# Optimization experiments

Hardware: AMD Instinct MI355X
Metric: run time of the kernel (lower is better)

The kernel has to match this reference:

```python
import jax, jax.numpy as jnp
import numpy as np

N_NODES = 100000


def _gcn_layer(h_in, W, b, src, dst, n_nodes):
    """PyG GCNConv: out = D^{-1/2} (A + I) D^{-1/2} (h_in @ W) + b.
    src/dst already include self-loops. Messages flow src -> dst."""
    h = h_in @ W  # [N, C_out]
    ones = jnp.ones(dst.shape[0], dtype=h.dtype)
    deg = jax.ops.segment_sum(ones, dst, num_segments=n_nodes)  # in-degree incl. self-loops
    dinv = jnp.where(deg > 0, jax.lax.rsqrt(deg), 0.0)
    norm = dinv[src] * dinv[dst]  # [E]
    msg = norm[:, None] * h[src]  # gather + scale, [E, C_out]
    out = jax.ops.segment_sum(msg, dst, num_segments=n_nodes)
    return out + b


def setup_inputs() -> dict:
    key = jax.random.key(0)
    ks = jax.random.split(key, 4)
    d_in, d_hid = 64, 64
    n_edges = 1600000
    x = jax.random.normal(ks[0], (N_NODES, d_in), dtype=jnp.float32)
    edge_index = jax.random.randint(ks[1], (2, n_edges), 0, N_NODES, dtype=jnp.int64)
    W1 = jax.random.normal(ks[2], (d_in, d_hid), dtype=jnp.float32) * (1.0 / np.sqrt(d_in))
    b1 = jnp.zeros((d_hid,), dtype=jnp.float32)
    W2 = jax.random.normal(ks[3], (d_hid, d_hid), dtype=jnp.float32) * (1.0 / np.sqrt(d_hid))
    b2 = jnp.zeros((d_hid,), dtype=jnp.float32)
    return {"x": x, "edge_index": edge_index, "W1": W1, "b1": b1, "W2": W2, "b2": b2}


def reference(x, edge_index, W1, b1, W2, b2):
    n = x.shape[0]
    loop = jnp.arange(n, dtype=edge_index.dtype)
    src = jnp.concatenate([edge_index[0], loop])  # add self-loops once, reused by both layers
    dst = jnp.concatenate([edge_index[1], loop])
    h = jax.nn.relu(_gcn_layer(x, W1, b1, src, dst, n))
    h = jax.nn.relu(_gcn_layer(h, W2, b2, src, dst, n))
    return h
```

## Files before the change

### kernel.cpp

```cpp
#include <hip/hip_runtime.h>
#include <hip/hip_bf16.h>


#define NDIM 64
#define BSHIFT 9
#define BNODES (1 << BSHIFT)
#define BCAP 10240
#define CHUNK 4096
#define CAPC 64
#define CSHIFT 6
#define MAXCHUNK 512
#define PHASES 13
#define PSHIFT 13

typedef float v2f __attribute__((ext_vector_type(2)));
typedef __attribute__((ext_vector_type(8))) short short8b;
typedef __attribute__((ext_vector_type(4))) float f32x4;

__device__ __forceinline__ unsigned f2bf_rne(float f) {
  unsigned u = __float_as_uint(f);
  return (u + 0x7fffu + ((u >> 16) & 1u)) >> 16;
}

__global__ __launch_bounds__(256) void bin_scatter_kernel(
    const int* __restrict__ src, const int* __restrict__ dst,
    unsigned* __restrict__ binned, int* __restrict__ cnt,
    int nedges, int nchunk, int nbuck) {
  __shared__ int lcnt[256], lbase[256], lcur[256], tscan[256];
  __shared__ int2 stage[CHUNK];
  const int t = threadIdx.x;
  const int c = blockIdx.x;
  const int i0 = c * CHUNK;
  int iend = i0 + CHUNK; if (iend > nedges) iend = nedges;
  lcnt[t] = 0;
  __syncthreads();
  for (int i = i0 + t; i < iend; i += 256)
    atomicAdd(&lcnt[dst[i] >> BSHIFT], 1);
  __syncthreads();
  tscan[t] = lcnt[t];
  __syncthreads();
  for (int off = 1; off < 256; off <<= 1) {
    int tv = (t >= off) ? tscan[t - off] : 0;
    __syncthreads();
    tscan[t] += tv;
    __syncthreads();
  }
  lbase[t] = tscan[t] - lcnt[t];
  lcur[t] = lbase[t];
  __syncthreads();
  for (int i = i0 + t; i < iend; i += 256) {
    int s = src[i], d = dst[i];
    int p = atomicAdd(&lcur[d >> BSHIFT], 1);
    stage[p] = make_int2(s, d);
  }
  __syncthreads();
  const int m = iend - i0;
  for (int i = t; i < m; i += 256) {
    int2 pr = stage[i];
    int b = pr.y >> BSHIFT;
    int off = i - lbase[b];
    if (off < CAPC)
      binned[(((size_t)b * nchunk + c) << CSHIFT) + off] =
          (((unsigned)(pr.y & (BNODES - 1))) << 17) | (unsigned)pr.x;
  }
  if (t < nbuck) cnt[t * nchunk + c] = (lcnt[t] < CAPC) ? lcnt[t] : CAPC;
}

struct CsrSh {
  int deg[BNODES], rpl[BNODES], tscan[256], ccnt[MAXCHUNK];
  int pcnt[BNODES * PHASES];
};
union CsrGemmSh {
  CsrSh c;
  ushort g[4][16 * NDIM];
};

__global__ __launch_bounds__(256) void csr_gemm1_kernel(
    const unsigned* __restrict__ binned, const int* __restrict__ cnt,
    int* __restrict__ rowbeg, int* __restrict__ rowend,
    int* __restrict__ csr_src, float* __restrict__ dinv,
    const float* __restrict__ X, const float* __restrict__ W,
    ushort* __restrict__ hsb, int n, int nchunk) {
  __shared__ __align__(16) CsrGemmSh sh;
  const int b = blockIdx.x, t = threadIdx.x;
  const int node0 = b << BSHIFT;
  int ncnt = n - node0; if (ncnt > BNODES) ncnt = BNODES;
  const int e0 = b * BCAP;
  const size_t bbase = ((size_t)b * nchunk) << CSHIFT;
  const int nslot = nchunk << CSHIFT;

  for (int i = t; i < BNODES * PHASES; i += 256) sh.c.pcnt[i] = 0;
  for (int i = t; i < nchunk; i += 256) sh.c.ccnt[i] = cnt[b * nchunk + i];
  __syncthreads();
  for (int idx = t; idx < nslot; idx += 256) {
    if ((idx & (CAPC - 1)) < sh.c.ccnt[idx >> CSHIFT]) {
      unsigned u = binned[bbase + idx];
      atomicAdd(&sh.c.pcnt[(u >> 17) * PHASES + ((u & 0x1FFFFu) >> PSHIFT)], 1);
    }
  }
  __syncthreads();
  for (int i = t; i < BNODES; i += 256) {
    int s = 0;
#pragma unroll
    for (int p = 0; p < PHASES; ++p) {
      int c = sh.c.pcnt[i * PHASES + p];
      sh.c.pcnt[i * PHASES + p] = s;
      s += c;
    }
    sh.c.deg[i] = s;
  }
  __syncthreads();
  int d0 = sh.c.deg[2 * t], d1 = sh.c.deg[2 * t + 1];
  int ps = d0 + d1;
  sh.c.tscan[t] = ps;
  __syncthreads();
  for (int off = 1; off < 256; off <<= 1) {
    int tv = (t >= off) ? sh.c.tscan[t - off] : 0;
    __syncthreads();
    sh.c.tscan[t] += tv;
    __syncthreads();
  }
  int eb = sh.c.tscan[t] - ps;
  sh.c.rpl[2 * t] = eb;
  sh.c.rpl[2 * t + 1] = eb + d0;
  __syncthreads();
  for (int i = t; i < ncnt; i += 256) {
    rowbeg[node0 + i] = e0 + sh.c.rpl[i];
    rowend[node0 + i] = e0 + sh.c.rpl[i] + sh.c.deg[i];
    dinv[node0 + i] = rsqrtf((float)sh.c.deg[i] + 1.0f);
  }
  __syncthreads();
  for (int idx = t; idx < nslot; idx += 256) {
    if ((idx & (CAPC - 1)) < sh.c.ccnt[idx >> CSHIFT]) {
      unsigned u = binned[bbase + idx];
      int nd = u >> 17;
      int s = (int)(u & 0x1FFFFu);
      int pos = sh.c.rpl[nd] + atomicAdd(&sh.c.pcnt[nd * PHASES + (s >> PSHIFT)], 1);
      csr_src[e0 + pos] = s;
    }
  }
  __syncthreads();

  const int l = t & 63;
  const int wv = t >> 6;
  const int lrow = l & 15;
  const int kg = l >> 4;
  short8b Whi[4][2], Wlo[4][2];
#pragma unroll
  for (int ct = 0; ct < 4; ++ct) {
#pragma unroll
    for (int ks = 0; ks < 2; ++ks) {
      const int c = ct * 16 + lrow;
      const int k0 = ks * 32 + kg * 8;
#pragma unroll
      for (int i = 0; i < 8; ++i) {
        float w = W[(k0 + i) * NDIM + c];
        unsigned hb = f2bf_rne(w);
        float hf = __uint_as_float(hb << 16);
        Whi[ct][ks][i] = (short)hb;
        Wlo[ct][ks][i] = (short)f2bf_rne(w - hf);
      }
    }
  }
  const int ntile = (ncnt + 15) >> 4;
  for (int ti = wv; ti < ntile; ti += 4) {
    const int row0 = node0 + (ti << 4);
    const int r = row0 + lrow;
    short8b Ahi[2], Alo[2];
    const float4* Xf = (const float4*)X;
#pragma unroll
    for (int ks = 0; ks < 2; ++ks) {
      float4 xa = make_float4(0.f, 0.f, 0.f, 0.f);
      float4 xb = make_float4(0.f, 0.f, 0.f, 0.f);
      if (r < n) {
        xa = Xf[(size_t)r * 16 + ks * 8 + kg * 2];
        xb = Xf[(size_t)r * 16 + ks * 8 + kg * 2 + 1];
      }
      float xs[8] = {xa.x, xa.y, xa.z, xa.w, xb.x, xb.y, xb.z, xb.w};
#pragma unroll
      for (int i = 0; i < 8; ++i) {
        unsigned hb = f2bf_rne(xs[i]);
        float hf = __uint_as_float(hb << 16);
        Ahi[ks][i] = (short)hb;
        Alo[ks][i] = (short)f2bf_rne(xs[i] - hf);
      }
    }
    f32x4 acc[4];
#pragma unroll
    for (int ct = 0; ct < 4; ++ct) {
      f32x4 a = {0.f, 0.f, 0.f, 0.f};
#pragma unroll
      for (int ks = 0; ks < 2; ++ks) {
        a = __builtin_amdgcn_mfma_f32_16x16x32_bf16(Ahi[ks], Whi[ct][ks], a, 0, 0, 0);
        a = __builtin_amdgcn_mfma_f32_16x16x32_bf16(Ahi[ks], Wlo[ct][ks], a, 0, 0, 0);
        a = __builtin_amdgcn_mfma_f32_16x16x32_bf16(Alo[ks], Whi[ct][ks], a, 0, 0, 0);
      }
      acc[ct] = a;
    }
#pragma unroll
    for (int q = 0; q < 4; ++q) {
      const int rr = row0 + kg * 4 + q;
      const float di = (rr < n) ? dinv[rr] : 0.f;
#pragma unroll
      for (int ct = 0; ct < 4; ++ct)
        sh.g[wv][(kg * 4 + q) * NDIM + ct * 16 + lrow] =
            (ushort)f2bf_rne(acc[ct][q] * di);
    }
#pragma unroll
    for (int e = 0; e < 2; ++e) {
      const int idx = e * 64 + l;
      const int rw = idx >> 3;
      if (row0 + rw < n)
        ((uint4*)hsb)[(size_t)(row0 + rw) * 8 + (idx & 7)] =
            ((const uint4*)sh.g[wv])[idx];
    }
  }
}

__global__ __launch_bounds__(256) void gemm_mfma_bf16_kernel(
    const ushort* __restrict__ Xin, const float* __restrict__ W,
    const float* __restrict__ dinv, ushort* __restrict__ hsb, int nrows) {
  __shared__ __attribute__((aligned(16))) ushort stage[4][16 * NDIM];
  const int tid = threadIdx.x;
  const int l = tid & 63;
  const int wv = tid >> 6;
  const int lrow = l & 15;
  const int kg = l >> 4;

  short8b Whi[4][2], Wlo[4][2];
#pragma unroll
  for (int ct = 0; ct < 4; ++ct) {
#pragma unroll
    for (int ks = 0; ks < 2; ++ks) {
      const int c = ct * 16 + lrow;
      const int k0 = ks * 32 + kg * 8;
#pragma unroll
      for (int i = 0; i < 8; ++i) {
        float w = W[(k0 + i) * NDIM + c];
        unsigned hb = f2bf_rne(w);
        float hf = __uint_as_float(hb << 16);
        Whi[ct][ks][i] = (short)hb;
        Wlo[ct][ks][i] = (short)f2bf_rne(w - hf);
      }
    }
  }

  const int tiles = (nrows + 15) >> 4;
  for (int tb = blockIdx.x * 4; tb < tiles; tb += gridDim.x * 4) {
    const int t = tb + wv;
    const int row0 = t << 4;
    const int r = row0 + lrow;
    short8b Ahi[2];
    const uint4* Xb = (const uint4*)Xin;
#pragma unroll
    for (int ks = 0; ks < 2; ++ks) {
      uint4 q = make_uint4(0u, 0u, 0u, 0u);
      if (r < nrows) q = Xb[(size_t)r * 8 + ks * 4 + kg];
      union { uint4 u; short8b s; } cv; cv.u = q;
      Ahi[ks] = cv.s;
    }
    f32x4 acc[4];
#pragma unroll
    for (int ct = 0; ct < 4; ++ct) {
      f32x4 a = {0.f, 0.f, 0.f, 0.f};
#pragma unroll
      for (int ks = 0; ks < 2; ++ks) {
        a = __builtin_amdgcn_mfma_f32_16x16x32_bf16(Ahi[ks], Whi[ct][ks], a, 0, 0, 0);
        a = __builtin_amdgcn_mfma_f32_16x16x32_bf16(Ahi[ks], Wlo[ct][ks], a, 0, 0, 0);
      }
      acc[ct] = a;
    }
#pragma unroll
    for (int q = 0; q < 4; ++q) {
      const int rr = row0 + kg * 4 + q;
      const float di = (rr < nrows) ? dinv[rr] : 0.f;
#pragma unroll
      for (int ct = 0; ct < 4; ++ct)
        stage[wv][(kg * 4 + q) * NDIM + ct * 16 + lrow] =
            (ushort)f2bf_rne(acc[ct][q] * di);
    }
    __syncthreads();
#pragma unroll
    for (int e = 0; e < 2; ++e) {
      const int idx = e * 64 + l;
      const int rw = idx >> 3;
      if (row0 + rw < nrows)
        ((uint4*)hsb)[(size_t)(row0 + rw) * 8 + (idx & 7)] =
            ((const uint4*)stage[wv])[idx];
    }
    __syncthreads();
  }
}

__device__ __forceinline__ void add8(v2f* acc, uint4 q) {
  v2f a0, a1, a2, a3;
  a0.x = __uint_as_float(q.x << 16); a0.y = __uint_as_float(q.x & 0xffff0000u);
  a1.x = __uint_as_float(q.y << 16); a1.y = __uint_as_float(q.y & 0xffff0000u);
  a2.x = __uint_as_float(q.z << 16); a2.y = __uint_as_float(q.z & 0xffff0000u);
  a3.x = __uint_as_float(q.w << 16); a3.y = __uint_as_float(q.w & 0xffff0000u);
  acc[0] += a0; acc[1] += a1; acc[2] += a2; acc[3] += a3;
}

template <bool BF16OUT>
__global__ __launch_bounds__(256) void agg_epi_kernel(
    const int* __restrict__ rowbeg, const int* __restrict__ rowend,
    const int* __restrict__ csr_src, const uint4* __restrict__ hsb4,
    const float* __restrict__ dinv, const float4* __restrict__ b4,
    void* __restrict__ outp, int n) {
  const int l = threadIdx.x & 63;
  const int wv = threadIdx.x >> 6;
  const int ql = l & 15;
  const int sg = ql >> 3;
  const int g = ql & 7;
  const int node = blockIdx.x * 16 + wv * 4 + (l >> 4);
  const bool alive = node < n;
  const int nodec = alive ? node : 0;
  int beg = rowbeg[nodec], end = rowend[nodec];
  if (!alive) { beg = 0; end = 0; }
  const int deg = end - beg;
  int dmax = deg;
  dmax = max(dmax, __shfl_xor(dmax, 16));
  dmax = max(dmax, __shfl_xor(dmax, 32));

  v2f acc[4];
#pragma unroll
  for (int i = 0; i < 4; ++i) acc[i] = (v2f)(0.f);

  for (int base = 0; base < dmax; base += 16) {
    const int rem = deg - base;
    int eidx = (ql < rem) ? csr_src[beg + base + ql] : 0;
#pragma unroll
    for (int j = 0; j < 16; j += 2) {
      const int e = j + sg;
      int s = __shfl(eidx, (l & 48) + e);
      uint4 q = hsb4[(size_t)s * 8 + g];
      if (e < rem) add8(acc, q);
    }
  }
  if (sg == 0) add8(acc, hsb4[(size_t)nodec * 8 + g]);

  float a[8];
#pragma unroll
  for (int i = 0; i < 4; ++i) { a[2 * i] = acc[i].x; a[2 * i + 1] = acc[i].y; }
#pragma unroll
  for (int i = 0; i < 8; ++i) a[i] += __shfl_xor(a[i], 8);

  if (sg == 0 && alive) {
    float di = dinv[node];
    float4 bb0 = b4[2 * g], bb1 = b4[2 * g + 1];
    float o[8];
    o[0] = fmaxf(di * a[0] + bb0.x, 0.f);
    o[1] = fmaxf(di * a[1] + bb0.y, 0.f);
    o[2] = fmaxf(di * a[2] + bb0.z, 0.f);
    o[3] = fmaxf(di * a[3] + bb0.w, 0.f);
    o[4] = fmaxf(di * a[4] + bb1.x, 0.f);
    o[5] = fmaxf(di * a[5] + bb1.y, 0.f);
    o[6] = fmaxf(di * a[6] + bb1.z, 0.f);
    o[7] = fmaxf(di * a[7] + bb1.w, 0.f);
    if (BF16OUT) {
      uint4 wvv;
      wvv.x = f2bf_rne(o[0]) | (f2bf_rne(o[1]) << 16);
      wvv.y = f2bf_rne(o[2]) | (f2bf_rne(o[3]) << 16);
      wvv.z = f2bf_rne(o[4]) | (f2bf_rne(o[5]) << 16);
      wvv.w = f2bf_rne(o[6]) | (f2bf_rne(o[7]) << 16);
      ((uint4*)outp)[(size_t)node * 8 + g] = wvv;
    } else {
      float4 o0 = make_float4(o[0], o[1], o[2], o[3]);
      float4 o1 = make_float4(o[4], o[5], o[6], o[7]);
      ((float4*)outp)[(size_t)node * 16 + 2 * g] = o0;
      ((float4*)outp)[(size_t)node * 16 + 2 * g + 1] = o1;
    }
  }
}

extern "C" void kernel_launch(void* const* d_in, const int* in_sizes, int n_in,
                              void* d_out, int out_size, void* d_ws, size_t ws_size,
                              hipStream_t stream) {
  const float* x  = (const float*)d_in[0];
  const int* eidx = (const int*)d_in[1];
  const float* W1 = (const float*)d_in[2];
  const float* b1 = (const float*)d_in[3];
  const float* W2 = (const float*)d_in[4];
  const float* b2 = (const float*)d_in[5];
  float* out = (float*)d_out;

  const int N = in_sizes[0] / NDIM;
  const int E = in_sizes[1] / 2;
  const int* src = eidx;
  const int* dst = eidx + E;
  const int NV = N * NDIM;
  const int nbuck = (N + BNODES - 1) >> BSHIFT;
  const int nchunk = (E + CHUNK - 1) / CHUNK;

  auto al128 = [](size_t v) { return (v + 127) & ~(size_t)127; };
  char* w = (char*)d_ws;
  unsigned* binned = (unsigned*)w;  w += al128(((size_t)nbuck * nchunk) << (CSHIFT + 2));
  int*   cnt     = (int*)w;    w += al128((size_t)nbuck * nchunk * 4);
  int*   csr_src = (int*)w;    w += al128((size_t)nbuck * BCAP * 4);
  int*   rowbeg  = (int*)w;    w += al128((size_t)N * 4);
  int*   rowend  = (int*)w;    w += al128((size_t)N * 4);
  float* dinv    = (float*)w;  w += al128((size_t)N * 4);
  ushort* hsb = (ushort*)w;  w += al128((size_t)NV * 2);
  ushort* h2b = (ushort*)w;

  bin_scatter_kernel<<<nchunk, 256, 0, stream>>>(src, dst, binned, cnt,
                                                 E, nchunk, nbuck);
  csr_gemm1_kernel<<<nbuck, 256, 0, stream>>>(binned, cnt, rowbeg, rowend,
                                              csr_src, dinv, x, W1, hsb,
                                              N, nchunk);
  agg_epi_kernel<true><<<(N + 15) / 16, 256, 0, stream>>>(
      rowbeg, rowend, csr_src, (const uint4*)hsb, dinv, (const float4*)b1, h2b, N);
  gemm_mfma_bf16_kernel<<<512, 256, 0, stream>>>(h2b, W2, dinv, hsb, N);
  agg_epi_kernel<false><<<(N + 15) / 16, 256, 0, stream>>>(
      rowbeg, rowend, csr_src, (const uint4*)hsb, dinv, (const float4*)b2, out, N);
}
```

Before: 260.0 us.

## Fuse binning, CSR build and first GEMM into one cooperative kernel

Merges the bin-scatter kernel and the CSR+GEMM1 kernel into a single persistent cooperative kernel that uses grid-wide syncs between phases, which removes a kernel launch boundary. The CSR phase now walks each chunk's valid entries serially per thread rather than striding over every slot, and GEMM1 tiles are spread across the whole grid instead of one bucket per block. In exchange it adds two grid syncs and a grid sized to occupancy (at most 512 blocks), so the binning and CSR phases loop over chunks and buckets. The per-thread serial chunk loops may also load-balance worse than before.

```diff
diff --git a/kernel.cpp b/kernel.cpp
--- a/kernel.cpp
+++ b/kernel.cpp
@@ -1,5 +1,8 @@
 #include <hip/hip_runtime.h>
+#include <hip/hip_cooperative_groups.h>
 #include <hip/hip_bf16.h>
+
+namespace cg = cooperative_groups;
 
 
 #define NDIM 64
@@ -22,127 +25,135 @@
   return (u + 0x7fffu + ((u >> 16) & 1u)) >> 16;
 }
 
-__global__ __launch_bounds__(256) void bin_scatter_kernel(
-    const int* __restrict__ src, const int* __restrict__ dst,
-    unsigned* __restrict__ binned, int* __restrict__ cnt,
-    int nedges, int nchunk, int nbuck) {
-  __shared__ int lcnt[256], lbase[256], lcur[256], tscan[256];
-  __shared__ int2 stage[CHUNK];
-  const int t = threadIdx.x;
-  const int c = blockIdx.x;
-  const int i0 = c * CHUNK;
-  int iend = i0 + CHUNK; if (iend > nedges) iend = nedges;
-  lcnt[t] = 0;
-  __syncthreads();
-  for (int i = i0 + t; i < iend; i += 256)
-    atomicAdd(&lcnt[dst[i] >> BSHIFT], 1);
-  __syncthreads();
-  tscan[t] = lcnt[t];
-  __syncthreads();
-  for (int off = 1; off < 256; off <<= 1) {
-    int tv = (t >= off) ? tscan[t - off] : 0;
-    __syncthreads();
-    tscan[t] += tv;
-    __syncthreads();
-  }
-  lbase[t] = tscan[t] - lcnt[t];
-  lcur[t] = lbase[t];
-  __syncthreads();
-  for (int i = i0 + t; i < iend; i += 256) {
-    int s = src[i], d = dst[i];
-    int p = atomicAdd(&lcur[d >> BSHIFT], 1);
-    stage[p] = make_int2(s, d);
-  }
-  __syncthreads();
-  const int m = iend - i0;
-  for (int i = t; i < m; i += 256) {
-    int2 pr = stage[i];
-    int b = pr.y >> BSHIFT;
-    int off = i - lbase[b];
-    if (off < CAPC)
-      binned[(((size_t)b * nchunk + c) << CSHIFT) + off] =
-          (((unsigned)(pr.y & (BNODES - 1))) << 17) | (unsigned)pr.x;
-  }
-  if (t < nbuck) cnt[t * nchunk + c] = (lcnt[t] < CAPC) ? lcnt[t] : CAPC;
-}
-
+struct BinSh {
+  int lcnt[256], lbase[256], lcur[256], tscan[256];
+  int2 stage[CHUNK];
+};
 struct CsrSh {
   int deg[BNODES], rpl[BNODES], tscan[256], ccnt[MAXCHUNK];
   int pcnt[BNODES * PHASES];
 };
-union CsrGemmSh {
+union FrontSh {
+  BinSh b;
   CsrSh c;
   ushort g[4][16 * NDIM];
 };
 
-__global__ __launch_bounds__(256) void csr_gemm1_kernel(
-    const unsigned* __restrict__ binned, const int* __restrict__ cnt,
+__global__ __launch_bounds__(256) void front_kernel(
+    const int* __restrict__ src, const int* __restrict__ dst,
+    unsigned* __restrict__ binned, int* __restrict__ cnt,
     int* __restrict__ rowbeg, int* __restrict__ rowend,
     int* __restrict__ csr_src, float* __restrict__ dinv,
     const float* __restrict__ X, const float* __restrict__ W,
-    ushort* __restrict__ hsb, int n, int nchunk) {
-  __shared__ __align__(16) CsrGemmSh sh;
-  const int b = blockIdx.x, t = threadIdx.x;
-  const int node0 = b << BSHIFT;
-  int ncnt = n - node0; if (ncnt > BNODES) ncnt = BNODES;
-  const int e0 = b * BCAP;
-  const size_t bbase = ((size_t)b * nchunk) << CSHIFT;
-  const int nslot = nchunk << CSHIFT;
-
-  for (int i = t; i < BNODES * PHASES; i += 256) sh.c.pcnt[i] = 0;
-  for (int i = t; i < nchunk; i += 256) sh.c.ccnt[i] = cnt[b * nchunk + i];
-  __syncthreads();
-  for (int idx = t; idx < nslot; idx += 256) {
-    if ((idx & (CAPC - 1)) < sh.c.ccnt[idx >> CSHIFT]) {
-      unsigned u = binned[bbase + idx];
-      atomicAdd(&sh.c.pcnt[(u >> 17) * PHASES + ((u & 0x1FFFFu) >> PSHIFT)], 1);
-    }
-  }
-  __syncthreads();
-  for (int i = t; i < BNODES; i += 256) {
-    int s = 0;
-#pragma unroll
-    for (int p = 0; p < PHASES; ++p) {
-      int c = sh.c.pcnt[i * PHASES + p];
-      sh.c.pcnt[i * PHASES + p] = s;
-      s += c;
-    }
-    sh.c.deg[i] = s;
-  }
-  __syncthreads();
-  int d0 = sh.c.deg[2 * t], d1 = sh.c.deg[2 * t + 1];
-  int ps = d0 + d1;
-  sh.c.tscan[t] = ps;
-  __syncthreads();
-  for (int off = 1; off < 256; off <<= 1) {
-    int tv = (t >= off) ? sh.c.tscan[t - off] : 0;
-    __syncthreads();
-    sh.c.tscan[t] += tv;
-    __syncthreads();
-  }
-  int eb = sh.c.tscan[t] - ps;
-  sh.c.rpl[2 * t] = eb;
-  sh.c.rpl[2 * t + 1] = eb + d0;
-  __syncthreads();
-  for (int i = t; i < ncnt; i += 256) {
-    rowbeg[node0 + i] = e0 + sh.c.rpl[i];
-    rowend[node0 + i] = e0 + sh.c.rpl[i] + sh.c.deg[i];
-    dinv[node0 + i] = rsqrtf((float)sh.c.deg[i] + 1.0f);
-  }
-  __syncthreads();
-  for (int idx = t; idx < nslot; idx += 256) {
-    if ((idx & (CAPC - 1)) < sh.c.ccnt[idx >> CSHIFT]) {
-      unsigned u = binned[bbase + idx];
-      int nd = u >> 17;
-      int s = (int)(u & 0x1FFFFu);
-      int pos = sh.c.rpl[nd] + atomicAdd(&sh.c.pcnt[nd * PHASES + (s >> PSHIFT)], 1);
-      csr_src[e0 + pos] = s;
-    }
-  }
-  __syncthreads();
+    ushort* __restrict__ hsb, int n, int nedges, int nbuck, int nchunk) {
+  __shared__ __align__(16) FrontSh sh;
+  cg::grid_group grid = cg::this_grid();
+  const int t = threadIdx.x;
+
+  for (int c = blockIdx.x; c < nchunk; c += gridDim.x) {
+    const int i0 = c * CHUNK;
+    int iend = i0 + CHUNK; if (iend > nedges) iend = nedges;
+    sh.b.lcnt[t] = 0;
+    __syncthreads();
+    for (int i = i0 + t; i < iend; i += 256)
+      atomicAdd(&sh.b.lcnt[dst[i] >> BSHIFT], 1);
+    __syncthreads();
+    sh.b.tscan[t] = sh.b.lcnt[t];
+    __syncthreads();
+    for (int off = 1; off < 256; off <<= 1) {
+      int tv = (t >= off) ? sh.b.tscan[t - off] : 0;
+      __syncthreads();
+      sh.b.tscan[t] += tv;
+      __syncthreads();
+    }
+    sh.b.lbase[t] = sh.b.tscan[t] - sh.b.lcnt[t];
+    sh.b.lcur[t] = sh.b.lbase[t];
+    __syncthreads();
+    for (int i = i0 + t; i < iend; i += 256) {
+      int s = src[i], d = dst[i];
+      int p = atomicAdd(&sh.b.lcur[d >> BSHIFT], 1);
+      sh.b.stage[p] = make_int2(s, d);
+    }
+    __syncthreads();
+    const int m = iend - i0;
+    for (int i = t; i < m; i += 256) {
+      int2 pr = sh.b.stage[i];
+      int b = pr.y >> BSHIFT;
+      int off = i - sh.b.lbase[b];
+      if (off < CAPC)
+        binned[(((size_t)b * nchunk + c) << CSHIFT) + off] =
+            (((unsigned)(pr.y & (BNODES - 1))) << 17) | (unsigned)pr.x;
+    }
+    if (t < nbuck) cnt[t * nchunk + c] = (sh.b.lcnt[t] < CAPC) ? sh.b.lcnt[t] : CAPC;
+    __syncthreads();
+  }
+  grid.sync();
+
+  for (int b = blockIdx.x; b < nbuck; b += gridDim.x) {
+    const int node0 = b << BSHIFT;
+    int ncnt = n - node0; if (ncnt > BNODES) ncnt = BNODES;
+    const int e0 = b * BCAP;
+    const size_t bbase = ((size_t)b * nchunk) << CSHIFT;
+    for (int i = t; i < BNODES * PHASES; i += 256) sh.c.pcnt[i] = 0;
+    for (int i = t; i < nchunk; i += 256) sh.c.ccnt[i] = cnt[b * nchunk + i];
+    __syncthreads();
+    for (int c = t; c < nchunk; c += 256) {
+      const int ne = sh.c.ccnt[c];
+      const unsigned* p = binned + bbase + ((size_t)c << CSHIFT);
+      for (int i = 0; i < ne; ++i) {
+        unsigned u = p[i];
+        atomicAdd(&sh.c.pcnt[(u >> 17) * PHASES + ((u & 0x1FFFFu) >> PSHIFT)], 1);
+      }
+    }
+    __syncthreads();
+    for (int i = t; i < BNODES; i += 256) {
+      int s = 0;
+#pragma unroll
+      for (int p = 0; p < PHASES; ++p) {
+        int cv = sh.c.pcnt[i * PHASES + p];
+        sh.c.pcnt[i * PHASES + p] = s;
+        s += cv;
+      }
+      sh.c.deg[i] = s;
+    }
+    __syncthreads();
+    int d0 = sh.c.deg[2 * t], d1 = sh.c.deg[2 * t + 1];
+    int ps = d0 + d1;
+    sh.c.tscan[t] = ps;
+    __syncthreads();
+    for (int off = 1; off < 256; off <<= 1) {
+      int tv = (t >= off) ? sh.c.tscan[t - off] : 0;
+      __syncthreads();
+      sh.c.tscan[t] += tv;
+      __syncthreads();
+    }
+    int eb = sh.c.tscan[t] - ps;
+    sh.c.rpl[2 * t] = eb;
+    sh.c.rpl[2 * t + 1] = eb + d0;
+    __syncthreads();
+    for (int i = t; i < ncnt; i += 256) {
+      rowbeg[node0 + i] = e0 + sh.c.rpl[i];
+      rowend[node0 + i] = e0 + sh.c.rpl[i] + sh.c.deg[i];
+      dinv[node0 + i] = rsqrtf((float)sh.c.deg[i] + 1.0f);
+    }
+    __syncthreads();
+    for (int c = t; c < nchunk; c += 256) {
+      const int ne = sh.c.ccnt[c];
+      const unsigned* p = binned + bbase + ((size_t)c << CSHIFT);
+      for (int i = 0; i < ne; ++i) {
+        unsigned u = p[i];
+        int nd = u >> 17;
+        int s = (int)(u & 0x1FFFFu);
+        int pos = sh.c.rpl[nd] + atomicAdd(&sh.c.pcnt[nd * PHASES + (s >> PSHIFT)], 1);
+        csr_src[e0 + pos] = s;
+      }
+    }
+    __syncthreads();
+  }
+  grid.sync();
 
   const int l = t & 63;
-  const int wv = t >> 6;
+  const int wvq = t >> 6;
   const int lrow = l & 15;
   const int kg = l >> 4;
   short8b Whi[4][2], Wlo[4][2];
@@ -162,9 +173,9 @@
       }
     }
   }
-  const int ntile = (ncnt + 15) >> 4;
-  for (int ti = wv; ti < ntile; ti += 4) {
-    const int row0 = node0 + (ti << 4);
+  const int tiles = (n + 15) >> 4;
+  for (int ti = blockIdx.x * 4 + wvq; ti < tiles; ti += gridDim.x * 4) {
+    const int row0 = ti << 4;
     const int r = row0 + lrow;
     short8b Ahi[2], Alo[2];
     const float4* Xf = (const float4*)X;
@@ -203,7 +214,7 @@
       const float di = (rr < n) ? dinv[rr] : 0.f;
 #pragma unroll
       for (int ct = 0; ct < 4; ++ct)
-        sh.g[wv][(kg * 4 + q) * NDIM + ct * 16 + lrow] =
+        sh.g[wvq][(kg * 4 + q) * NDIM + ct * 16 + lrow] =
             (ushort)f2bf_rne(acc[ct][q] * di);
     }
 #pragma unroll
@@ -212,7 +223,7 @@
       const int rw = idx >> 3;
       if (row0 + rw < n)
         ((uint4*)hsb)[(size_t)(row0 + rw) * 8 + (idx & 7)] =
-            ((const uint4*)sh.g[wv])[idx];
+            ((const uint4*)sh.g[wvq])[idx];
     }
   }
 }
@@ -403,11 +414,35 @@
   ushort* hsb = (ushort*)w;  w += al128((size_t)NV * 2);
   ushort* h2b = (ushort*)w;
 
-  bin_scatter_kernel<<<nchunk, 256, 0, stream>>>(src, dst, binned, cnt,
-                                                 E, nchunk, nbuck);
-  csr_gemm1_kernel<<<nbuck, 256, 0, stream>>>(binned, cnt, rowbeg, rowend,
-                                              csr_src, dinv, x, W1, hsb,
-                                              N, nchunk);
+  static int nblk = 0;
+  if (nblk == 0) {
+    int perCU = 0;
+    hipOccupancyMaxActiveBlocksPerMultiprocessor(
+        &perCU, reinterpret_cast<const void*>(front_kernel), 256, 0);
+    if (perCU < 1) perCU = 1;
+    hipDeviceProp_t prop{};
+    int ncu = 256;
+    if (hipGetDeviceProperties(&prop, 0) == hipSuccess &&
+        prop.multiProcessorCount > 0)
+      ncu = prop.multiProcessorCount;
+    nblk = perCU * ncu;
+    if (nblk > 512) nblk = 512;
+  }
+
+  const int* p_src = src;  const int* p_dst = dst;
+  unsigned* p_binned = binned; int* p_cnt = cnt;
+  int* p_rowbeg = rowbeg;  int* p_rowend = rowend;
+  int* p_csr = csr_src;    float* p_dinv = dinv;
+  const float* p_x = x;    const float* p_W1 = W1;
+  ushort* p_hsb = hsb;
+  int p_n = N, p_e = E, p_nbuck = nbuck, p_nchunk = nchunk;
+  void* args[] = {&p_src, &p_dst, &p_binned, &p_cnt,
+                  &p_rowbeg, &p_rowend, &p_csr, &p_dinv,
+                  &p_x, &p_W1, &p_hsb,
+                  &p_n, &p_e, &p_nbuck, &p_nchunk};
+  hipLaunchCooperativeKernel(reinterpret_cast<const void*>(front_kernel),
+                             dim3(nblk), dim3(256), args, 0, stream);
+
   agg_epi_kernel<true><<<(N + 15) / 16, 256, 0, stream>>>(
       rowbeg, rowend, csr_src, (const uint4*)hsb, dinv, (const float4*)b1, h2b, N);
   gemm_mfma_bf16_kernel<<<512, 256, 0, stream>>>(h2b, W2, dinv, hsb, N);
```

Measured after the change: 316.7 us. 1.22x slower.
